# Kernel optimization log

Measured on AMD Instinct MI355X. Metric: run time of the kernel, lower is better.

## Reference

```python
import jax, jax.numpy as jnp
from jax import lax
import numpy as np

SEQ, FEAT, VOCAB = 59, 64, 578
B, U = 4096, 1024


def setup_inputs() -> dict:
    key = jax.random.key(0)
    ks = jax.random.split(key, 6)
    x = jax.random.normal(ks[0], (B, SEQ, FEAT), dtype=jnp.float32)
    # Keras LSTMCell params: kernel [feat, 4U], recurrent_kernel [U, 4U], bias [4U]
    kernel = jax.random.normal(ks[1], (FEAT, 4 * U), dtype=jnp.float32) * 0.05
    rec_kernel = jax.random.normal(ks[2], (U, 4 * U), dtype=jnp.float32) * 0.05
    bias = jnp.zeros((4 * U,), dtype=jnp.float32)
    w2 = jax.random.normal(ks[3], (U, VOCAB), dtype=jnp.float32) * 0.05
    b2 = jnp.zeros((VOCAB,), dtype=jnp.float32)
    return {"x": x, "kernel": kernel, "rec_kernel": rec_kernel, "bias": bias, "w2": w2, "b2": b2}


def reference(x, kernel, rec_kernel, bias, w2, b2):
    batch = x.shape[0]
    units = rec_kernel.shape[0]
    xs = jnp.transpose(x, (1, 0, 2))  # [SEQ, B, FEAT]
    h0 = jnp.zeros((batch, units), dtype=x.dtype)
    c0 = jnp.zeros((batch, units), dtype=x.dtype)

    def step(carry, xt):
        h, c = carry
        z = xt @ kernel + h @ rec_kernel + bias  # [B, 4U]
        i, f, g, o = jnp.split(z, 4, axis=-1)    # Keras gate order i,f,c,o
        i = jax.nn.sigmoid(i)
        f = jax.nn.sigmoid(f)
        g = jnp.tanh(g)
        o = jax.nn.sigmoid(o)
        c_new = f * c + i * g
        h_new = o * jnp.tanh(c_new)
        return (h_new, c_new), None

    (h_last, _), _ = lax.scan(step, (h0, c0), xs)
    probs = jax.nn.softmax(h_last @ w2 + b2, axis=-1)  # dense2 softmax on last hidden
    # original: stack single prediction -> [1,B,V], transpose [1,0,2] -> [B,1,V]
    return probs[:, None, :]
```

## Files before the change

### kernel.cpp

```cpp
#include <hip/hip_runtime.h>

#define SEQ    59
#define FEAT   64
#define VOCAB  578
#define BATCH  4096
#define UNITS  1024
#define KLSTM  1088
#define NPAD   640

typedef __bf16 bf16x8 __attribute__((ext_vector_type(8)));
typedef __bf16 bf16x4 __attribute__((ext_vector_type(4)));
typedef float  floatx4 __attribute__((ext_vector_type(4)));

typedef const __attribute__((address_space(1))) char gas_char;
typedef __attribute__((address_space(3))) char las_char;

__device__ __forceinline__ float sigmoid_f(float x) { return 1.f / (1.f + __expf(-x)); }
__device__ __forceinline__ float tanh_f(float x) { float e = __expf(2.f * x); return 1.f - 2.f / (e + 1.f); }


__global__ void convert_x_kernel(const float* __restrict__ x, __bf16* __restrict__ xbf) {
    int i = blockIdx.x * 256 + threadIdx.x;
    const int total = BATCH * SEQ * FEAT / 4;
    if (i >= total) return;
    float4 v = ((const float4*)x)[i];
    bf16x4 o;
    o.x = (__bf16)v.x; o.y = (__bf16)v.y; o.z = (__bf16)v.z; o.w = (__bf16)v.w;
    ((bf16x4*)xbf)[i] = o;
}

__global__ void convert_weights_kernel(const float* __restrict__ kern,
                                       const float* __restrict__ reck,
                                       __bf16* __restrict__ Wtp) {
    int idx = blockIdx.x * 256 + threadIdx.x;
    if (idx >= 4096 * KLSTM) return;
    int np = idx / KLSTM;
    int k  = idx - np * KLSTM;
    int ublk = np >> 7;
    int g    = (np >> 5) & 3;
    int j    = np & 31;
    int n    = g * 1024 + ublk * 32 + j;
    float v = (k < FEAT) ? kern[(size_t)k * 4096 + n]
                         : reck[(size_t)(k - FEAT) * 4096 + n];
    Wtp[idx] = (__bf16)v;
}

__global__ void convert_w2_kernel(const float* __restrict__ w2, __bf16* __restrict__ Wt2p) {
    int idx = blockIdx.x * 256 + threadIdx.x;
    if (idx >= NPAD * 1024) return;
    int n = idx >> 10;
    int k = idx & 1023;
    float v = (n < VOCAB) ? w2[(size_t)k * VOCAB + n] : 0.f;
    Wt2p[idx] = (__bf16)v;
}

__global__ void __launch_bounds__(256, 2) lstm_step_kernel(
    const __bf16* __restrict__ xbf,
    const __bf16* __restrict__ Wtp,
    const float*  __restrict__ bias,
    const __bf16* __restrict__ hin,
    __bf16*       __restrict__ hout,
    float*        __restrict__ cstate,
    int t)
{
    __shared__ __bf16 As[128 * 64];
    __shared__ __bf16 Bs[2][128 * 64];

    const int tid  = threadIdx.x;
    const int wid  = tid >> 6;
    const int lane = tid & 63;
    const int ln   = lane & 15;
    const int lk   = lane >> 4;
    const int wm   = wid >> 1;
    const int wn   = wid & 1;
    const int rb   = blockIdx.x;
    const int yb   = blockIdx.y;

    floatx4 acc[2][4][4];
#pragma unroll
    for (int p = 0; p < 2; ++p)
#pragma unroll
        for (int m = 0; m < 4; ++m)
#pragma unroll
            for (int g = 0; g < 4; ++g)
                acc[p][m][g] = (floatx4){0.f, 0.f, 0.f, 0.f};

    int s_row[4], s_kgd[4];
#pragma unroll
    for (int q = 0; q < 4; ++q) {
        int flat = q * 256 + tid;
        int row  = flat >> 3;
        s_row[q] = row;
        s_kgd[q] = (flat & 7) ^ (row & 7);
    }

    for (int kt = 0; kt < 17; ++kt) {
        __syncthreads();
#pragma unroll
        for (int q = 0; q < 4; ++q) {
            const int row = s_row[q], kgd = s_kgd[q];
            const __bf16* gp;
            if (kt == 0)
                gp = xbf + (size_t)(rb * 128 + row) * (SEQ * FEAT) + t * FEAT + kgd * 8;
            else
                gp = hin + ((size_t)(rb * 128 + row) << 10) + (kt - 1) * 64 + kgd * 8;
            __builtin_amdgcn_global_load_lds((gas_char*)gp,
                (las_char*)(As + (size_t)(q * 256 + (wid << 6)) * 8), 16, 0, 0);
        }
#pragma unroll
        for (int p = 0; p < 2; ++p) {
#pragma unroll
            for (int q = 0; q < 4; ++q) {
                const int n = s_row[q], kgd = s_kgd[q];
                const __bf16* gp = Wtp + (size_t)(yb * 256 + p * 128 + n) * KLSTM + kt * 64 + kgd * 8;
                __builtin_amdgcn_global_load_lds((gas_char*)gp,
                    (las_char*)(Bs[p] + (size_t)(q * 256 + (wid << 6)) * 8), 16, 0, 0);
            }
        }
        __syncthreads();
#pragma unroll
        for (int kk = 0; kk < 2; ++kk) {
            const int kg = kk * 4 + lk;
            bf16x8 a[4], b0[4], b1[4];
#pragma unroll
            for (int m = 0; m < 4; ++m) {
                int row  = wm * 64 + m * 16 + ln;
                int ccol = (kg ^ (row & 7)) * 8;
                a[m] = *(const bf16x8*)(As + row * 64 + ccol);
            }
#pragma unroll
            for (int g = 0; g < 4; ++g) {
                int n    = g * 32 + wn * 16 + ln;
                int ccol = (kg ^ (n & 7)) * 8;
                b0[g] = *(const bf16x8*)(Bs[0] + n * 64 + ccol);
                b1[g] = *(const bf16x8*)(Bs[1] + n * 64 + ccol);
            }
#pragma unroll
            for (int m = 0; m < 4; ++m)
#pragma unroll
                for (int g = 0; g < 4; ++g) {
                    acc[0][m][g] = __builtin_amdgcn_mfma_f32_16x16x32_bf16(a[m], b0[g], acc[0][m][g], 0, 0, 0);
                    acc[1][m][g] = __builtin_amdgcn_mfma_f32_16x16x32_bf16(a[m], b1[g], acc[1][m][g], 0, 0, 0);
                }
        }
    }

#pragma unroll
    for (int p = 0; p < 2; ++p) {
        const int u  = (yb * 2 + p) * 32 + wn * 16 + ln;
        const float bi  = bias[u];
        const float bfv = bias[UNITS + u];
        const float bg  = bias[2 * UNITS + u];
        const float bo  = bias[3 * UNITS + u];
#pragma unroll
        for (int m = 0; m < 4; ++m) {
            const int row0 = rb * 128 + wm * 64 + m * 16 + lk * 4;
#pragma unroll
            for (int r = 0; r < 4; ++r) {
                const size_t idx = ((size_t)(row0 + r) << 10) + u;
                float ig = sigmoid_f(acc[p][m][0][r] + bi);
                float fg = sigmoid_f(acc[p][m][1][r] + bfv);
                float gg = tanh_f(acc[p][m][2][r] + bg);
                float og = sigmoid_f(acc[p][m][3][r] + bo);
                float cn = fg * cstate[idx] + ig * gg;
                cstate[idx] = cn;
                hout[idx] = (__bf16)(og * tanh_f(cn));
            }
        }
    }
}

__global__ void __launch_bounds__(256) dense_kernel(
    const __bf16* __restrict__ hin,
    const __bf16* __restrict__ Wt2p,
    float*        __restrict__ logits)
{
    __shared__ __bf16 As[128 * 64];
    __shared__ __bf16 Bs[128 * 64];

    const int tid  = threadIdx.x;
    const int wid  = tid >> 6;
    const int lane = tid & 63;
    const int ln   = lane & 15;
    const int lk   = lane >> 4;
    const int wm   = wid >> 1;
    const int wn   = wid & 1;
    const int rb   = blockIdx.x;
    const int nb   = blockIdx.y;

    floatx4 acc[4][4];
#pragma unroll
    for (int m = 0; m < 4; ++m)
#pragma unroll
        for (int g = 0; g < 4; ++g)
            acc[m][g] = (floatx4){0.f, 0.f, 0.f, 0.f};

    int s_row[4], s_kgd[4];
#pragma unroll
    for (int q = 0; q < 4; ++q) {
        int flat = q * 256 + tid;
        int row  = flat >> 3;
        s_row[q] = row;
        s_kgd[q] = (flat & 7) ^ (row & 7);
    }

    for (int kt = 0; kt < 16; ++kt) {
        __syncthreads();
#pragma unroll
        for (int q = 0; q < 4; ++q) {
            const int row = s_row[q], kgd = s_kgd[q];
            const __bf16* gp = hin + ((size_t)(rb * 128 + row) << 10) + kt * 64 + kgd * 8;
            __builtin_amdgcn_global_load_lds((gas_char*)gp,
                (las_char*)(As + (size_t)(q * 256 + (wid << 6)) * 8), 16, 0, 0);
        }
#pragma unroll
        for (int q = 0; q < 4; ++q) {
            const int n = s_row[q], kgd = s_kgd[q];
            const __bf16* gp = Wt2p + ((size_t)(nb * 128 + n) << 10) + kt * 64 + kgd * 8;
            __builtin_amdgcn_global_load_lds((gas_char*)gp,
                (las_char*)(Bs + (size_t)(q * 256 + (wid << 6)) * 8), 16, 0, 0);
        }
        __syncthreads();
#pragma unroll
        for (int kk = 0; kk < 2; ++kk) {
            const int kg = kk * 4 + lk;
            bf16x8 a[4], b[4];
#pragma unroll
            for (int m = 0; m < 4; ++m) {
                int row  = wm * 64 + m * 16 + ln;
                int ccol = (kg ^ (row & 7)) * 8;
                a[m] = *(const bf16x8*)(As + row * 64 + ccol);
            }
#pragma unroll
            for (int g = 0; g < 4; ++g) {
                int n    = g * 32 + wn * 16 + ln;
                int ccol = (kg ^ (n & 7)) * 8;
                b[g] = *(const bf16x8*)(Bs + n * 64 + ccol);
            }
#pragma unroll
            for (int m = 0; m < 4; ++m)
#pragma unroll
                for (int g = 0; g < 4; ++g)
                    acc[m][g] = __builtin_amdgcn_mfma_f32_16x16x32_bf16(a[m], b[g], acc[m][g], 0, 0, 0);
        }
    }

#pragma unroll
    for (int m = 0; m < 4; ++m) {
        const int row0 = rb * 128 + wm * 64 + m * 16 + lk * 4;
#pragma unroll
        for (int g = 0; g < 4; ++g) {
            const int n = nb * 128 + g * 32 + wn * 16 + ln;
#pragma unroll
            for (int r = 0; r < 4; ++r)
                logits[(size_t)(row0 + r) * NPAD + n] = acc[m][g][r];
        }
    }
}

__global__ void __launch_bounds__(256) softmax_kernel(
    const float* __restrict__ logits,
    const float* __restrict__ b2,
    float* __restrict__ out)
{
    const int row = blockIdx.x;
    const int tid = threadIdx.x;
    __shared__ float red[8];

    float z[3];
    float lmax = -1e30f;
#pragma unroll
    for (int j = 0; j < 3; ++j) {
        int col = tid + j * 256;
        if (col < VOCAB) {
            z[j] = logits[(size_t)row * NPAD + col] + b2[col];
            lmax = fmaxf(lmax, z[j]);
        } else z[j] = -1e30f;
    }
    for (int off = 32; off > 0; off >>= 1) lmax = fmaxf(lmax, __shfl_xor(lmax, off));
    if ((tid & 63) == 0) red[tid >> 6] = lmax;
    __syncthreads();
    lmax = fmaxf(fmaxf(red[0], red[1]), fmaxf(red[2], red[3]));
    __syncthreads();

    float lsum = 0.f;
#pragma unroll
    for (int j = 0; j < 3; ++j) {
        int col = tid + j * 256;
        if (col < VOCAB) { z[j] = __expf(z[j] - lmax); lsum += z[j]; }
    }
    for (int off = 32; off > 0; off >>= 1) lsum += __shfl_xor(lsum, off);
    if ((tid & 63) == 0) red[tid >> 6] = lsum;
    __syncthreads();
    lsum = red[0] + red[1] + red[2] + red[3];
    float inv = 1.f / lsum;
#pragma unroll
    for (int j = 0; j < 3; ++j) {
        int col = tid + j * 256;
        if (col < VOCAB) out[(size_t)row * VOCAB + col] = z[j] * inv;
    }
}

extern "C" void kernel_launch(void* const* d_in, const int* in_sizes, int n_in,
                              void* d_out, int out_size, void* d_ws, size_t ws_size,
                              hipStream_t stream)
{
    const float* x    = (const float*)d_in[0];
    const float* kern = (const float*)d_in[1];
    const float* reck = (const float*)d_in[2];
    const float* bias = (const float*)d_in[3];
    const float* w2   = (const float*)d_in[4];
    const float* b2   = (const float*)d_in[5];
    float* out = (float*)d_out;

    char* ws = (char*)d_ws;
    size_t off = 0;
    auto alloc = [&](size_t bytes) {
        char* p = ws + off;
        off += (bytes + 255) & ~(size_t)255;
        return p;
    };
    __bf16* Wtp    = (__bf16*)alloc((size_t)4096 * KLSTM * 2);
    __bf16* Wt2p   = (__bf16*)alloc((size_t)NPAD * 1024 * 2);
    __bf16* xbf    = (__bf16*)alloc((size_t)BATCH * SEQ * FEAT * 2);
    __bf16* h0     = (__bf16*)alloc((size_t)BATCH * UNITS * 2);
    __bf16* h1     = (__bf16*)alloc((size_t)BATCH * UNITS * 2);
    float*  cst    = (float*)alloc((size_t)BATCH * UNITS * 4);
    float*  logits = (float*)alloc((size_t)BATCH * NPAD * 4);
    if (off > ws_size) return;

    (void)hipMemsetAsync(h0, 0, (size_t)BATCH * UNITS * 2, stream);
    (void)hipMemsetAsync(cst, 0, (size_t)BATCH * UNITS * 4, stream);

    convert_x_kernel<<<(BATCH * SEQ * FEAT / 4 + 255) / 256, 256, 0, stream>>>(x, xbf);
    convert_weights_kernel<<<(4096 * KLSTM + 255) / 256, 256, 0, stream>>>(kern, reck, Wtp);
    convert_w2_kernel<<<(NPAD * 1024 + 255) / 256, 256, 0, stream>>>(w2, Wt2p);

    __bf16* hin = h0; __bf16* hout = h1;
    for (int t = 0; t < SEQ; ++t) {
        lstm_step_kernel<<<dim3(32, 16), 256, 0, stream>>>(xbf, Wtp, bias, hin, hout, cst, t);
        __bf16* tmp = hin; hin = hout; hout = tmp;
    }

    dense_kernel<<<dim3(32, 5), 256, 0, stream>>>(hin, Wt2p, logits);
    softmax_kernel<<<BATCH, 256, 0, stream>>>(logits, b2, out);
}
```

Baseline: 2.578 ms.

## Enlarge LSTM step tile to 256x256 with double-buffered LDS K-loop

Each LSTM step block now handles 256 batch rows by 256 gate columns with 512 threads on a 1D grid of 256 blocks, instead of 128x256 with 256 threads. The K loop becomes double-buffered in 128 KB of dynamic LDS: the next x/h and weight chunks are loaded while the current chunk is fed to MFMAs, with one barrier per iteration. The aim is to overlap global-to-LDS transfers with matrix math and to halve the number of weight-tile reloads per row block. The cost is that the LDS footprint allows only one block per CU, which cuts latency hiding from co-resident blocks.

```diff
diff --git a/kernel.cpp b/kernel.cpp
--- a/kernel.cpp
+++ b/kernel.cpp
@@ -54,7 +54,7 @@
     Wt2p[idx] = (__bf16)v;
 }
 
-__global__ void __launch_bounds__(256, 2) lstm_step_kernel(
+__global__ void __launch_bounds__(512, 2) lstm_step_kernel(
     const __bf16* __restrict__ xbf,
     const __bf16* __restrict__ Wtp,
     const float*  __restrict__ bias,
@@ -63,8 +63,9 @@
     float*        __restrict__ cstate,
     int t)
 {
-    __shared__ __bf16 As[128 * 64];
-    __shared__ __bf16 Bs[2][128 * 64];
+    extern __shared__ __bf16 smem[];
+    __bf16* As = smem;
+    __bf16* Bs = smem + 32768;
 
     const int tid  = threadIdx.x;
     const int wid  = tid >> 6;
@@ -73,95 +74,144 @@
     const int lk   = lane >> 4;
     const int wm   = wid >> 1;
     const int wn   = wid & 1;
-    const int rb   = blockIdx.x;
-    const int yb   = blockIdx.y;
-
-    floatx4 acc[2][4][4];
-#pragma unroll
-    for (int p = 0; p < 2; ++p)
-#pragma unroll
-        for (int m = 0; m < 4; ++m)
-#pragma unroll
-            for (int g = 0; g < 4; ++g)
-                acc[p][m][g] = (floatx4){0.f, 0.f, 0.f, 0.f};
+    const int bid  = blockIdx.x;
+    const int yb   = bid & 15;
+    const int rb   = bid >> 4;
 
     int s_row[4], s_kgd[4];
 #pragma unroll
     for (int q = 0; q < 4; ++q) {
-        int flat = q * 256 + tid;
+        int flat = q * 512 + tid;
         int row  = flat >> 3;
         s_row[q] = row;
         s_kgd[q] = (flat & 7) ^ (row & 7);
     }
 
-    for (int kt = 0; kt < 17; ++kt) {
+    floatx4 acc[4][4][2];
+#pragma unroll
+    for (int m = 0; m < 4; ++m)
+#pragma unroll
+        for (int g = 0; g < 4; ++g)
+#pragma unroll
+            for (int h = 0; h < 2; ++h)
+                acc[m][g][h] = (floatx4){0.f, 0.f, 0.f, 0.f};
+
+#pragma unroll
+    for (int q = 0; q < 4; ++q) {
+        const int row = s_row[q], kgd = s_kgd[q];
+        const __bf16* gp = xbf + (size_t)(rb * 256 + row) * (SEQ * FEAT) + t * FEAT + kgd * 8;
+        __builtin_amdgcn_global_load_lds((gas_char*)gp,
+            (las_char*)(As + (size_t)(q * 512 + (wid << 6)) * 8), 16, 0, 0);
+    }
+#pragma unroll
+    for (int q = 0; q < 4; ++q) {
+        const int n = s_row[q], kgd = s_kgd[q];
+        const __bf16* gp = Wtp + (size_t)(yb * 256 + n) * KLSTM + kgd * 8;
+        __builtin_amdgcn_global_load_lds((gas_char*)gp,
+            (las_char*)(Bs + (size_t)(q * 512 + (wid << 6)) * 8), 16, 0, 0);
+    }
+
+#pragma unroll 1
+    for (int kt = 0; kt < 16; ++kt) {
+        const int cb = kt & 1;
+        const int sb = cb ^ 1;
         __syncthreads();
+
 #pragma unroll
         for (int q = 0; q < 4; ++q) {
             const int row = s_row[q], kgd = s_kgd[q];
-            const __bf16* gp;
-            if (kt == 0)
-                gp = xbf + (size_t)(rb * 128 + row) * (SEQ * FEAT) + t * FEAT + kgd * 8;
-            else
-                gp = hin + ((size_t)(rb * 128 + row) << 10) + (kt - 1) * 64 + kgd * 8;
+            const __bf16* gp = hin + ((size_t)(rb * 256 + row) << 10) + kt * 64 + kgd * 8;
             __builtin_amdgcn_global_load_lds((gas_char*)gp,
-                (las_char*)(As + (size_t)(q * 256 + (wid << 6)) * 8), 16, 0, 0);
-        }
-#pragma unroll
-        for (int p = 0; p < 2; ++p) {
-#pragma unroll
-            for (int q = 0; q < 4; ++q) {
-                const int n = s_row[q], kgd = s_kgd[q];
-                const __bf16* gp = Wtp + (size_t)(yb * 256 + p * 128 + n) * KLSTM + kt * 64 + kgd * 8;
-                __builtin_amdgcn_global_load_lds((gas_char*)gp,
-                    (las_char*)(Bs[p] + (size_t)(q * 256 + (wid << 6)) * 8), 16, 0, 0);
-            }
-        }
-        __syncthreads();
+                (las_char*)(As + sb * 16384 + (size_t)(q * 512 + (wid << 6)) * 8), 16, 0, 0);
+        }
+#pragma unroll
+        for (int q = 0; q < 4; ++q) {
+            const int n = s_row[q], kgd = s_kgd[q];
+            const __bf16* gp = Wtp + (size_t)(yb * 256 + n) * KLSTM + (kt + 1) * 64 + kgd * 8;
+            __builtin_amdgcn_global_load_lds((gas_char*)gp,
+                (las_char*)(Bs + sb * 16384 + (size_t)(q * 512 + (wid << 6)) * 8), 16, 0, 0);
+        }
+
+        const __bf16* Ab = As + cb * 16384;
+        const __bf16* Bb = Bs + cb * 16384;
 #pragma unroll
         for (int kk = 0; kk < 2; ++kk) {
             const int kg = kk * 4 + lk;
-            bf16x8 a[4], b0[4], b1[4];
+            bf16x8 a[4], b[4][2];
 #pragma unroll
             for (int m = 0; m < 4; ++m) {
                 int row  = wm * 64 + m * 16 + ln;
                 int ccol = (kg ^ (row & 7)) * 8;
-                a[m] = *(const bf16x8*)(As + row * 64 + ccol);
+                a[m] = *(const bf16x8*)(Ab + row * 64 + ccol);
             }
 #pragma unroll
-            for (int g = 0; g < 4; ++g) {
-                int n    = g * 32 + wn * 16 + ln;
-                int ccol = (kg ^ (n & 7)) * 8;
-                b0[g] = *(const bf16x8*)(Bs[0] + n * 64 + ccol);
-                b1[g] = *(const bf16x8*)(Bs[1] + n * 64 + ccol);
+            for (int g = 0; g < 4; ++g)
+#pragma unroll
+                for (int h = 0; h < 2; ++h) {
+                    int n    = wn * 128 + g * 32 + h * 16 + ln;
+                    int ccol = (kg ^ (n & 7)) * 8;
+                    b[g][h] = *(const bf16x8*)(Bb + n * 64 + ccol);
+                }
+#pragma unroll
+            for (int m = 0; m < 4; ++m)
+#pragma unroll
+                for (int g = 0; g < 4; ++g)
+#pragma unroll
+                    for (int h = 0; h < 2; ++h)
+                        acc[m][g][h] = __builtin_amdgcn_mfma_f32_16x16x32_bf16(a[m], b[g][h], acc[m][g][h], 0, 0, 0);
+        }
+    }
+
+    {
+        __syncthreads();
+        const __bf16* Ab = As;
+        const __bf16* Bb = Bs;
+#pragma unroll
+        for (int kk = 0; kk < 2; ++kk) {
+            const int kg = kk * 4 + lk;
+            bf16x8 a[4], b[4][2];
+#pragma unroll
+            for (int m = 0; m < 4; ++m) {
+                int row  = wm * 64 + m * 16 + ln;
+                int ccol = (kg ^ (row & 7)) * 8;
+                a[m] = *(const bf16x8*)(Ab + row * 64 + ccol);
             }
 #pragma unroll
+            for (int g = 0; g < 4; ++g)
+#pragma unroll
+                for (int h = 0; h < 2; ++h) {
+                    int n    = wn * 128 + g * 32 + h * 16 + ln;
+                    int ccol = (kg ^ (n & 7)) * 8;
+                    b[g][h] = *(const bf16x8*)(Bb + n * 64 + ccol);
+                }
+#pragma unroll
             for (int m = 0; m < 4; ++m)
 #pragma unroll
-                for (int g = 0; g < 4; ++g) {
-                    acc[0][m][g] = __builtin_amdgcn_mfma_f32_16x16x32_bf16(a[m], b0[g], acc[0][m][g], 0, 0, 0);
-                    acc[1][m][g] = __builtin_amdgcn_mfma_f32_16x16x32_bf16(a[m], b1[g], acc[1][m][g], 0, 0, 0);
-                }
-        }
-    }
-
-#pragma unroll
-    for (int p = 0; p < 2; ++p) {
-        const int u  = (yb * 2 + p) * 32 + wn * 16 + ln;
+                for (int g = 0; g < 4; ++g)
+#pragma unroll
+                    for (int h = 0; h < 2; ++h)
+                        acc[m][g][h] = __builtin_amdgcn_mfma_f32_16x16x32_bf16(a[m], b[g][h], acc[m][g][h], 0, 0, 0);
+        }
+    }
+
+    const int ublk = yb * 2 + wn;
+#pragma unroll
+    for (int h = 0; h < 2; ++h) {
+        const int u  = ublk * 32 + h * 16 + ln;
         const float bi  = bias[u];
         const float bfv = bias[UNITS + u];
         const float bg  = bias[2 * UNITS + u];
         const float bo  = bias[3 * UNITS + u];
 #pragma unroll
         for (int m = 0; m < 4; ++m) {
-            const int row0 = rb * 128 + wm * 64 + m * 16 + lk * 4;
+            const int row0 = rb * 256 + wm * 64 + m * 16 + lk * 4;
 #pragma unroll
             for (int r = 0; r < 4; ++r) {
                 const size_t idx = ((size_t)(row0 + r) << 10) + u;
-                float ig = sigmoid_f(acc[p][m][0][r] + bi);
-                float fg = sigmoid_f(acc[p][m][1][r] + bfv);
-                float gg = tanh_f(acc[p][m][2][r] + bg);
-                float og = sigmoid_f(acc[p][m][3][r] + bo);
+                float ig = sigmoid_f(acc[m][0][h][r] + bi);
+                float fg = sigmoid_f(acc[m][1][h][r] + bfv);
+                float gg = tanh_f(acc[m][2][h][r] + bg);
+                float og = sigmoid_f(acc[m][3][h][r] + bo);
                 float cn = fg * cstate[idx] + ig * gg;
                 cstate[idx] = cn;
                 hout[idx] = (__bf16)(og * tanh_f(cn));
@@ -329,6 +379,9 @@
     float*  logits = (float*)alloc((size_t)BATCH * NPAD * 4);
     if (off > ws_size) return;
 
+    (void)hipFuncSetAttribute((const void*)lstm_step_kernel,
+                              hipFuncAttributeMaxDynamicSharedMemorySize, 128 * 1024);
+
     (void)hipMemsetAsync(h0, 0, (size_t)BATCH * UNITS * 2, stream);
     (void)hipMemsetAsync(cst, 0, (size_t)BATCH * UNITS * 4, stream);
 
@@ -338,7 +391,7 @@
 
     __bf16* hin = h0; __bf16* hout = h1;
     for (int t = 0; t < SEQ; ++t) {
-        lstm_step_kernel<<<dim3(32, 16), 256, 0, stream>>>(xbf, Wtp, bias, hin, hout, cst, t);
+        lstm_step_kernel<<<256, 512, 128 * 1024, stream>>>(xbf, Wtp, bias, hin, hout, cst, t);
         __bf16* tmp = hin; hin = hout; hout = tmp;
     }
 
```

New measurement: 2.690 ms. 4.4% more time.
